# Optimization experiments

Hardware: AMD Instinct MI355X
Metric: run time of the kernel (lower is better)

Reference implementation:

```python
import jax, jax.numpy as jnp
import numpy as np

B, D, H, W = 64, 256, 32, 32
K, DC = 1024, 128  # codebook size, codebook dim = D // 2
BETA = 0.25


def setup_inputs() -> dict:
    key = jax.random.key(0)
    ks = jax.random.split(key, 4)
    return {
        "x": jax.random.normal(ks[0], (B, D, H, W), dtype=jnp.float32),
        "pre_W": jax.random.normal(ks[1], (DC, D), dtype=jnp.float32) * (1.0 / np.sqrt(D)),
        "pre_b": jnp.zeros((DC,), dtype=jnp.float32),
        "post_W": jax.random.normal(ks[2], (D, DC), dtype=jnp.float32) * (1.0 / np.sqrt(DC)),
        "post_b": jnp.zeros((D,), dtype=jnp.float32),
        "lookup_table": jax.random.normal(ks[3], (K, DC), dtype=jnp.float32) * (1.0 / np.sqrt(DC)),
    }


def reference(x, pre_W, pre_b, post_W, post_b, lookup_table):
    sg = jax.lax.stop_gradient
    b, d, h, w = x.shape
    # pre-quant 1x1 conv: [b, d, h, w] -> [b, dc, h, w]
    z = jnp.einsum("bchw,oc->bohw", x, pre_W) + pre_b[None, :, None, None]
    # flatten tokens: [b*h*w, dc]
    zf = z.transpose(0, 2, 3, 1).reshape(-1, DC)
    # squared distances to codebook (argmin identical to cdist argmin)
    d2 = (
        jnp.sum(zf * zf, axis=1, keepdims=True)
        - 2.0 * zf @ lookup_table.T
        + jnp.sum(lookup_table * lookup_table, axis=1)[None, :]
    )  # [N, K]
    q = jnp.argmin(d2, axis=1)  # [N]
    x_e = lookup_table[q].reshape(b, h, w, DC).transpose(0, 3, 1, 2)  # [b, dc, h, w]
    # losses (enable_ema_update = False path)
    codebook_loss = jnp.mean((sg(z) - x_e) ** 2)
    commitment_loss = BETA * jnp.mean((z - sg(x_e)) ** 2)
    loss = (1.0 - BETA) * codebook_loss + commitment_loss
    # straight-through estimator
    z_st = z + sg(x_e - z)
    # post-quant 1x1 conv: [b, dc, h, w] -> [b, d, h, w]
    out = jnp.einsum("bchw,oc->bohw", z_st, post_W) + post_b[None, :, None, None]
    # perplexity from empirical code usage
    counts = jnp.zeros((K,), dtype=jnp.float32).at[q].add(1.0)
    e_mean = counts / q.shape[0]
    perplexity = jnp.exp(-jnp.sum(e_mean * jnp.log(e_mean + 1e-10)))
    q_map = q.reshape(b, h, w)
    return out, loss, q_map, perplexity
```

## Files before the change

kernel.cpp:

```cpp
#include <hip/hip_runtime.h>
#include <cstdint>

#define NB   64
#define ND   256
#define NHW  1024
#define NTOK 65536
#define NDC  128
#define NK   1024

#define OFF_LOSS 16777216
#define OFF_Q    16777217
#define OFF_PERP 16842753

#define GAPTHR 1e-3f
#define NEGINF (-3.402823466e38f)

typedef short short8 __attribute__((ext_vector_type(8)));
typedef float f32x4 __attribute__((ext_vector_type(4)));

__device__ __forceinline__ unsigned short f2bf(float f) {
  unsigned u = __float_as_uint(f);
  u += 0x7FFFu + ((u >> 16) & 1u);
  return (unsigned short)(u >> 16);
}
__device__ __forceinline__ float bf2f(unsigned short h) {
  return __uint_as_float(((unsigned)h) << 16);
}

__device__ __forceinline__ void gll16(const void* g, void* l) {
  __builtin_amdgcn_global_load_lds(
      (const __attribute__((address_space(1))) unsigned int*)g,
      (__attribute__((address_space(3))) unsigned int*)l, 16, 0, 0);
}

__global__ __launch_bounds__(256) void k_init(
    const float* __restrict__ lut, const float* __restrict__ preW,
    const float* __restrict__ postW,
    unsigned short* __restrict__ ch,
    unsigned short* __restrict__ pwh, unsigned short* __restrict__ pwl,
    unsigned short* __restrict__ qwh, unsigned short* __restrict__ qwl,
    float* __restrict__ nhn, double* __restrict__ cn2d,
    int* __restrict__ counts, double* __restrict__ lossAcc, int* __restrict__ ctr) {
  int tid = blockIdx.x * 256 + threadIdx.x;
  int stride = gridDim.x * 256;
  for (int i = tid; i < NK * NDC; i += stride) {
    int code = i >> 7, c = i & 127;
    float f = lut[i];
    unsigned short h1 = f2bf(f);
    float r = f - bf2f(h1);
    ch[code * 256 + c] = h1;
    ch[code * 256 + 128 + c] = f2bf(r);
  }
  for (int i = tid; i < NDC * ND; i += stride) {
    float f = preW[i];
    unsigned u = __float_as_uint(f);
    float lf = f - __uint_as_float(u & 0xffff0000u);
    pwh[i] = (unsigned short)(u >> 16);
    pwl[i] = (unsigned short)(__float_as_uint(lf) >> 16);
  }
  for (int i = tid; i < ND * NDC; i += stride) {
    float f = postW[i];
    unsigned u = __float_as_uint(f);
    float lf = f - __uint_as_float(u & 0xffff0000u);
    qwh[i] = (unsigned short)(u >> 16);
    qwl[i] = (unsigned short)(__float_as_uint(lf) >> 16);
  }
  if (tid < NK) {
    float s = 0.f;
    double sd = 0.0;
    for (int c = 0; c < NDC; c++) {
      float v = lut[tid * NDC + c];
      s = fmaf(v, v, s);
      sd = fma((double)v, (double)v, sd);
    }
    nhn[tid] = -0.5f * s;
    cn2d[tid] = sd;
    counts[tid] = 0;
  }
  if (tid == 0) { *lossAcc = 0.0; *ctr = 0; }
}

__global__ __launch_bounds__(256, 3) void k_preconv(
    const float* __restrict__ x, const unsigned short* __restrict__ pwh,
    const unsigned short* __restrict__ pwl, const float* __restrict__ pre_b,
    float* __restrict__ zf) {
  int bx = blockIdx.x;
  int b = bx >> 4, p0 = (bx & 15) * 64;
  int tid = threadIdx.x;
  int lane = tid & 63, w = tid >> 6;
  int g = lane >> 4, l15 = lane & 15;
  int p = p0 + w * 16 + l15;
  const float* xb = x + (size_t)b * (ND * NHW) + p;

  float xv[64];
  #pragma unroll
  for (int c = 0; c < 8; ++c)
    #pragma unroll
    for (int j = 0; j < 8; ++j)
      xv[c * 8 + j] = xb[(size_t)(c * 32 + g * 8 + j) * NHW];

  f32x4 acc[8];
  #pragma unroll
  for (int rt = 0; rt < 8; ++rt) acc[rt] = (f32x4){0.f, 0.f, 0.f, 0.f};

  #pragma unroll
  for (int c = 0; c < 8; ++c) {
    int k0 = c * 32;
    short8 bh, bl;
    #pragma unroll
    for (int j = 0; j < 8; ++j) {
      float f = xv[c * 8 + j];
      unsigned u = __float_as_uint(f);
      float lf = f - __uint_as_float(u & 0xffff0000u);
      bh[j] = (short)(u >> 16);
      bl[j] = (short)(__float_as_uint(lf) >> 16);
    }
    #pragma unroll
    for (int rt = 0; rt < 8; ++rt) {
      short8 ah = *reinterpret_cast<const short8*>(&pwh[(rt * 16 + l15) * ND + k0 + g * 8]);
      short8 al = *reinterpret_cast<const short8*>(&pwl[(rt * 16 + l15) * ND + k0 + g * 8]);
      acc[rt] = __builtin_amdgcn_mfma_f32_16x16x32_bf16(ah, bh, acc[rt], 0, 0, 0);
      acc[rt] = __builtin_amdgcn_mfma_f32_16x16x32_bf16(ah, bl, acc[rt], 0, 0, 0);
      acc[rt] = __builtin_amdgcn_mfma_f32_16x16x32_bf16(al, bh, acc[rt], 0, 0, 0);
    }
  }
  int n = bx * 64 + w * 16 + l15;
  #pragma unroll
  for (int rt = 0; rt < 8; ++rt) {
    float4 bb = *reinterpret_cast<const float4*>(&pre_b[rt * 16 + g * 4]);
    float4 v;
    v.x = acc[rt][0] + bb.x;
    v.y = acc[rt][1] + bb.y;
    v.z = acc[rt][2] + bb.z;
    v.w = acc[rt][3] + bb.w;
    *reinterpret_cast<float4*>(&zf[(size_t)n * NDC + rt * 16 + g * 4]) = v;
  }
}

__global__ __launch_bounds__(256, 2) void k_dist(
    const float* __restrict__ zf, const unsigned short* __restrict__ ch,
    const float* __restrict__ nhn,
    int* __restrict__ q, int* __restrict__ list, int* __restrict__ ctr,
    double* __restrict__ lossAcc) {
  __shared__ __align__(16) short chbuf[2][16384];
  __shared__ float HnLds[NK];
  __shared__ float zn2Lds[4][2][16];
  __shared__ float red[256];
  int tid = threadIdx.x;
  int lane = tid & 63, w = tid >> 6;
  int g = lane >> 4;
  int n0 = blockIdx.x * 128;

  for (int i = tid; i < NK; i += 256) HnLds[i] = nhn[i];

  short8 az[2][8];
  {
    int arow = lane & 15;
    #pragma unroll
    for (int rt = 0; rt < 2; ++rt) {
      const float* zr = zf + (size_t)(n0 + w * 32 + rt * 16 + arow) * NDC;
      float sq = 0.f;
      #pragma unroll
      for (int f = 0; f < 4; ++f) {
        const float* p = zr + f * 32 + g * 8;
        float4 v0 = *reinterpret_cast<const float4*>(p);
        float4 v1 = *reinterpret_cast<const float4*>(p + 4);
        float vv[8] = {v0.x, v0.y, v0.z, v0.w, v1.x, v1.y, v1.z, v1.w};
        short8 hi, lo;
        #pragma unroll
        for (int j = 0; j < 8; ++j) {
          sq = fmaf(vv[j], vv[j], sq);
          unsigned short h1 = f2bf(vv[j]);
          float r = vv[j] - bf2f(h1);
          hi[j] = (short)h1;
          lo[j] = (short)f2bf(r);
        }
        az[rt][f] = hi;
        az[rt][4 + f] = lo;
      }
      sq += __shfl_xor(sq, 16, 64);
      sq += __shfl_xor(sq, 32, 64);
      if (g == 0) zn2Lds[w][rt][arow] = sq;
    }
  }

  float best[2][4], sec[2][4];
  int bidx[2][4];
  #pragma unroll
  for (int rt = 0; rt < 2; ++rt)
    #pragma unroll
    for (int r = 0; r < 4; ++r) { best[rt][r] = NEGINF; sec[rt][r] = NEGINF; bidx[rt][r] = 0; }

  const char* chg = (const char*)ch;
  {
    const char* gb = chg + 0;
    #pragma unroll
    for (int rr = 0; rr < 8; ++rr) {
      int o = rr * 4096 + tid * 16;
      int so = o ^ (((o >> 9) & 7) << 4);
      gll16(gb + so, ((char*)&chbuf[0][0]) + o);
    }
  }
  asm volatile("s_waitcnt vmcnt(0)" ::: "memory");
  __syncthreads();

  int cur = 0;
  for (int chunk = 0; chunk < 16; ++chunk) {
    if (chunk < 15) {
      const char* gb = chg + (chunk + 1) * 32768;
      #pragma unroll
      for (int rr = 0; rr < 8; ++rr) {
        int o = rr * 4096 + tid * 16;
        int so = o ^ (((o >> 9) & 7) << 4);
        gll16(gb + so, ((char*)&chbuf[cur ^ 1][0]) + o);
      }
    }
    const char* cb = (const char*)&chbuf[cur][0];
    for (int ct = 0; ct < 4; ++ct) {
      int codeg = chunk * 64 + ct * 16 + (lane & 15);
      float nh = HnLds[codeg];
      short8 bc[8];
      #pragma unroll
      for (int f = 0; f < 8; ++f) {
        int byte = ((lane & 15) + ct * 16) * 512 + f * 64 + g * 16;
        byte ^= ((lane & 7) << 4);
        bc[f] = *reinterpret_cast<const short8*>(cb + byte);
      }
      f32x4 acc0 = {nh, nh, nh, nh};
      f32x4 acc1 = {nh, nh, nh, nh};
      #pragma unroll
      for (int j = 0; j < 4; ++j) {
        acc0 = __builtin_amdgcn_mfma_f32_16x16x32_bf16(az[0][j], bc[j], acc0, 0, 0, 0);
        acc1 = __builtin_amdgcn_mfma_f32_16x16x32_bf16(az[1][j], bc[j], acc1, 0, 0, 0);
        acc0 = __builtin_amdgcn_mfma_f32_16x16x32_bf16(az[0][j], bc[4 + j], acc0, 0, 0, 0);
        acc1 = __builtin_amdgcn_mfma_f32_16x16x32_bf16(az[1][j], bc[4 + j], acc1, 0, 0, 0);
        acc0 = __builtin_amdgcn_mfma_f32_16x16x32_bf16(az[0][4 + j], bc[j], acc0, 0, 0, 0);
        acc1 = __builtin_amdgcn_mfma_f32_16x16x32_bf16(az[1][4 + j], bc[j], acc1, 0, 0, 0);
      }
      #pragma unroll
      for (int r = 0; r < 4; ++r) {
        float s0 = acc0[r];
        bool t0 = s0 > best[0][r];
        bidx[0][r] = t0 ? codeg : bidx[0][r];
        sec[0][r] = fmaxf(sec[0][r], fminf(s0, best[0][r]));
        best[0][r] = fmaxf(s0, best[0][r]);
        float s1 = acc1[r];
        bool t1 = s1 > best[1][r];
        bidx[1][r] = t1 ? codeg : bidx[1][r];
        sec[1][r] = fmaxf(sec[1][r], fminf(s1, best[1][r]));
        best[1][r] = fmaxf(s1, best[1][r]);
      }
    }
    asm volatile("s_waitcnt vmcnt(0)" ::: "memory");
    __syncthreads();
    cur ^= 1;
  }

  float lsum = 0.f;
  #pragma unroll
  for (int rt = 0; rt < 2; ++rt) {
    #pragma unroll
    for (int r = 0; r < 4; ++r) {
      float b = best[rt][r];
      float s2 = sec[rt][r];
      int bi_ = bidx[rt][r];
      #pragma unroll
      for (int m = 1; m < 16; m <<= 1) {
        float ob = __shfl_xor(b, m, 64);
        float os = __shfl_xor(s2, m, 64);
        int oi = __shfl_xor(bi_, m, 64);
        float ns = fmaxf(fmaxf(s2, os), fminf(b, ob));
        bool take = (ob > b) || (ob == b && oi < bi_);
        b = take ? ob : b;
        bi_ = take ? oi : bi_;
        s2 = ns;
      }
      if ((lane & 15) == 0) {
        int token = n0 + w * 32 + rt * 16 + g * 4 + r;
        q[token] = bi_;
        if (b - s2 < GAPTHR) {
          int pos = atomicAdd(ctr, 1);
          list[pos] = token;
        }
        lsum += zn2Lds[w][rt][g * 4 + r] - 2.0f * b;
      }
    }
  }
  red[tid] = lsum;
  __syncthreads();
  for (int s = 128; s > 0; s >>= 1) {
    if (tid < s) red[tid] += red[tid + s];
    __syncthreads();
  }
  if (tid == 0) atomicAdd(lossAcc, (double)red[0]);
}

__global__ __launch_bounds__(256) void k_rescore(
    const float* __restrict__ x, const float* __restrict__ preW,
    const float* __restrict__ pre_b, const float* __restrict__ lut,
    const double* __restrict__ cn2d,
    const int* __restrict__ list, const int* __restrict__ ctr, int* __restrict__ q) {
  __shared__ float xs[4][256];
  __shared__ double zs[4][128];
  __shared__ double rd[4][256];
  __shared__ int    rc[4][256];
  int nf = *ctr;
  int tid = threadIdx.x;
  int w = tid >> 6, lane = tid & 63;
  for (int g0 = blockIdx.x * 4; g0 < nf; g0 += gridDim.x * 4) {
    int nt = nf - g0; if (nt > 4) nt = 4;
    #pragma unroll
    for (int t = 0; t < 4; ++t) {
      int token = list[g0 + (t < nt ? t : 0)];
      int b = token >> 10, p = token & 1023;
      xs[t][tid] = x[(size_t)(b * ND + tid) * NHW + p];
    }
    __syncthreads();
    #pragma unroll
    for (int rep = 0; rep < 2; ++rep) {
      int idx = rep * 256 + tid;
      int t = idx >> 7, dc = idx & 127;
      double acc = (double)pre_b[dc];
      const float* wr = preW + (size_t)dc * ND;
      #pragma unroll 4
      for (int d = 0; d < ND; d += 4) {
        float4 wv = *reinterpret_cast<const float4*>(wr + d);
        acc = fma((double)wv.x, (double)xs[t][d + 0], acc);
        acc = fma((double)wv.y, (double)xs[t][d + 1], acc);
        acc = fma((double)wv.z, (double)xs[t][d + 2], acc);
        acc = fma((double)wv.w, (double)xs[t][d + 3], acc);
      }
      zs[t][dc] = acc;
    }
    __syncthreads();
    double bd[4]; int bc_[4];
    #pragma unroll
    for (int t = 0; t < 4; ++t) { bd[t] = 1e300; bc_[t] = 0x7fffffff; }
    for (int cc = 0; cc < 4; ++cc) {
      int c = cc * 256 + tid;
      const float* cr = lut + (size_t)c * NDC;
      double a0 = 0.0, a1 = 0.0, a2 = 0.0, a3 = 0.0;
      #pragma unroll 4
      for (int k = 0; k < NDC; ++k) {
        double lc = (double)cr[k];
        a0 = fma(zs[0][k], lc, a0);
        a1 = fma(zs[1][k], lc, a1);
        a2 = fma(zs[2][k], lc, a2);
        a3 = fma(zs[3][k], lc, a3);
      }
      double cn = cn2d[c];
      double d0 = cn - 2.0 * a0; if (d0 < bd[0]) { bd[0] = d0; bc_[0] = c; }
      double d1 = cn - 2.0 * a1; if (d1 < bd[1]) { bd[1] = d1; bc_[1] = c; }
      double d2 = cn - 2.0 * a2; if (d2 < bd[2]) { bd[2] = d2; bc_[2] = c; }
      double d3 = cn - 2.0 * a3; if (d3 < bd[3]) { bd[3] = d3; bc_[3] = c; }
    }
    #pragma unroll
    for (int t = 0; t < 4; ++t) { rd[t][tid] = bd[t]; rc[t][tid] = bc_[t]; }
    __syncthreads();
    {
      double b_ = rd[w][lane]; int c_ = rc[w][lane];
      #pragma unroll
      for (int s = 64; s < 256; s += 64) {
        double ob = rd[w][lane + s]; int oc = rc[w][lane + s];
        if (ob < b_ || (ob == b_ && oc < c_)) { b_ = ob; c_ = oc; }
      }
      #pragma unroll
      for (int m = 1; m < 64; m <<= 1) {
        double ob = __shfl_xor(b_, m, 64);
        int oc = __shfl_xor(c_, m, 64);
        if (ob < b_ || (ob == b_ && oc < c_)) { b_ = ob; c_ = oc; }
      }
      if (lane == 0 && w < nt) q[list[g0 + w]] = c_;
    }
    __syncthreads();
  }
}

__global__ __launch_bounds__(256, 3) void k_post(
    const float* __restrict__ lut,
    const int* __restrict__ q, const unsigned short* __restrict__ qwh,
    const unsigned short* __restrict__ qwl, const float* __restrict__ post_b,
    float* __restrict__ out,
    int* __restrict__ counts, float* __restrict__ outq) {
  int bx = blockIdx.x;
  int n0 = (bx >> 1) * 128;
  int oh = (bx & 1) * 128;
  int b = n0 >> 10, p0 = n0 & 1023;
  int tid = threadIdx.x;
  int lane = tid & 63, w = tid >> 6;
  int g = lane >> 4, l15 = lane & 15;

  int qv[2];
  #pragma unroll
  for (int ct = 0; ct < 2; ++ct) qv[ct] = q[n0 + w * 32 + ct * 16 + l15];

  float4 ga[2][4][2];
  #pragma unroll
  for (int ct = 0; ct < 2; ++ct) {
    const float* xr0 = lut + (size_t)qv[ct] * NDC + g * 8;
    #pragma unroll
    for (int ks = 0; ks < 4; ++ks) {
      ga[ct][ks][0] = *reinterpret_cast<const float4*>(xr0 + ks * 32);
      ga[ct][ks][1] = *reinterpret_cast<const float4*>(xr0 + ks * 32 + 4);
    }
  }

  if (tid < 64) {
    int n = n0 + ((bx & 1) << 6) + tid;
    int c = q[n];
    atomicAdd(&counts[c], 1);
    outq[n] = (float)c;
  }

  short8 ah[2][4], al[2][4];
  #pragma unroll
  for (int ct = 0; ct < 2; ++ct)
    #pragma unroll
    for (int ks = 0; ks < 4; ++ks) {
      float vv[8] = {ga[ct][ks][0].x, ga[ct][ks][0].y, ga[ct][ks][0].z, ga[ct][ks][0].w,
                     ga[ct][ks][1].x, ga[ct][ks][1].y, ga[ct][ks][1].z, ga[ct][ks][1].w};
      #pragma unroll
      for (int j = 0; j < 8; ++j) {
        unsigned u = __float_as_uint(vv[j]);
        float lf = vv[j] - __uint_as_float(u & 0xffff0000u);
        ah[ct][ks][j] = (short)(u >> 16);
        al[ct][ks][j] = (short)(__float_as_uint(lf) >> 16);
      }
    }

  f32x4 acc[8][2];
  #pragma unroll
  for (int nt = 0; nt < 8; ++nt)
    #pragma unroll
    for (int ct = 0; ct < 2; ++ct) acc[nt][ct] = (f32x4){0.f, 0.f, 0.f, 0.f};

  #pragma unroll
  for (int ks = 0; ks < 4; ++ks) {
    int k0 = ks * 32;
    #pragma unroll
    for (int nt = 0; nt < 8; ++nt) {
      short8 bh = *reinterpret_cast<const short8*>(&qwh[(size_t)(oh + nt * 16 + l15) * NDC + k0 + g * 8]);
      short8 bl = *reinterpret_cast<const short8*>(&qwl[(size_t)(oh + nt * 16 + l15) * NDC + k0 + g * 8]);
      #pragma unroll
      for (int ct = 0; ct < 2; ++ct) {
        acc[nt][ct] = __builtin_amdgcn_mfma_f32_16x16x32_bf16(ah[ct][ks], bh, acc[nt][ct], 0, 0, 0);
        acc[nt][ct] = __builtin_amdgcn_mfma_f32_16x16x32_bf16(al[ct][ks], bh, acc[nt][ct], 0, 0, 0);
        acc[nt][ct] = __builtin_amdgcn_mfma_f32_16x16x32_bf16(ah[ct][ks], bl, acc[nt][ct], 0, 0, 0);
      }
    }
  }
  #pragma unroll
  for (int nt = 0; nt < 8; ++nt) {
    int o = oh + nt * 16 + l15;
    float bias = post_b[o];
    float* orow = out + (size_t)(b * ND + o) * NHW;
    #pragma unroll
    for (int ct = 0; ct < 2; ++ct) {
      int p = p0 + w * 32 + ct * 16 + g * 4;
      float4 v;
      v.x = acc[nt][ct][0] + bias;
      v.y = acc[nt][ct][1] + bias;
      v.z = acc[nt][ct][2] + bias;
      v.w = acc[nt][ct][3] + bias;
      *reinterpret_cast<float4*>(orow + p) = v;
    }
  }
}

__global__ __launch_bounds__(256) void k_fin(
    const double* __restrict__ lossAcc, const int* __restrict__ counts,
    float* __restrict__ out_loss, float* __restrict__ out_perp) {
  __shared__ float red[256];
  int tid = threadIdx.x;
  float h = 0.f;
  for (int i = tid; i < NK; i += 256) {
    float e = (float)counts[i] * (1.0f / (float)NTOK);
    h += e * logf(e + 1e-10f);
  }
  red[tid] = h;
  __syncthreads();
  for (int s = 128; s > 0; s >>= 1) {
    if (tid < s) red[tid] += red[tid + s];
    __syncthreads();
  }
  if (tid == 0) {
    *out_perp = expf(-red[0]);
    *out_loss = (float)(*lossAcc / ((double)NTOK * (double)NDC));
  }
}

extern "C" void kernel_launch(void* const* d_in, const int* in_sizes, int n_in,
                              void* d_out, int out_size, void* d_ws, size_t ws_size,
                              hipStream_t stream) {
  const float* x     = (const float*)d_in[0];
  const float* preW  = (const float*)d_in[1];
  const float* preb  = (const float*)d_in[2];
  const float* postW = (const float*)d_in[3];
  const float* postb = (const float*)d_in[4];
  const float* lut   = (const float*)d_in[5];
  float* out = (float*)d_out;

  char* ws = (char*)d_ws;
  float*          zf      = (float*)(ws);
  unsigned short* ch      = (unsigned short*)(ws + 33554432);
  unsigned short* pwh     = (unsigned short*)(ws + 34078720);
  unsigned short* pwl     = (unsigned short*)(ws + 34144256);
  unsigned short* qwh     = (unsigned short*)(ws + 34209792);
  unsigned short* qwl     = (unsigned short*)(ws + 34275328);
  float*          nhn     = (float*)(ws + 34340864);
  int*            q       = (int*)  (ws + 34344960);
  int*            list    = (int*)  (ws + 34607104);
  int*            counts  = (int*)  (ws + 34869248);
  double*         lossAcc = (double*)(ws + 34873344);
  int*            ctr     = (int*)  (ws + 34873352);
  double*         cn2d    = (double*)(ws + 34873360);

  float* out_loss = out + OFF_LOSS;
  float* out_q    = out + OFF_Q;
  float* out_perp = out + OFF_PERP;

  hipLaunchKernelGGL(k_init, dim3(512), dim3(256), 0, stream,
                     lut, preW, postW, ch, pwh, pwl, qwh, qwl, nhn, cn2d,
                     counts, lossAcc, ctr);
  hipLaunchKernelGGL(k_preconv, dim3(1024), dim3(256), 0, stream, x, pwh, pwl, preb, zf);
  hipLaunchKernelGGL(k_dist, dim3(512), dim3(256), 0, stream, zf, ch, nhn, q, list, ctr, lossAcc);
  hipLaunchKernelGGL(k_rescore, dim3(1024), dim3(256), 0, stream,
                     x, preW, preb, lut, cn2d, list, ctr, q);
  hipLaunchKernelGGL(k_post, dim3(1024), dim3(256), 0, stream,
                     lut, q, qwh, qwl, postb, out, counts, out_q);
  hipLaunchKernelGGL(k_fin, dim3(1), dim3(256), 0, stream, lossAcc, counts, out_loss, out_perp);
}
```

Baseline: 222.2 us.

## Tile preconv over 256 tokens with double-buffered LDS staging of x

Rewrites the pre-quant 1x1 conv so each block handles 256 tokens instead of 64. The x slices are staged through double-buffered, swizzled shared memory using direct global-to-LDS loads, and the next channel chunk is prefetched while MFMAs run on the current one. Each loaded weight fragment now feeds four token tiles, which cuts redundant weight reads. In exchange the grid drops from 1024 to 256 blocks at occupancy 1 on a chip with many CUs, and the 32 accumulator tiles raise register pressure.

```diff
diff --git a/kernel.cpp b/kernel.cpp
--- a/kernel.cpp
+++ b/kernel.cpp
@@ -80,60 +80,90 @@
   if (tid == 0) { *lossAcc = 0.0; *ctr = 0; }
 }
 
-__global__ __launch_bounds__(256, 3) void k_preconv(
+__global__ __launch_bounds__(256, 1) void k_preconv(
     const float* __restrict__ x, const unsigned short* __restrict__ pwh,
     const unsigned short* __restrict__ pwl, const float* __restrict__ pre_b,
     float* __restrict__ zf) {
+  __shared__ __align__(16) float xs[2][32 * 256];
   int bx = blockIdx.x;
-  int b = bx >> 4, p0 = (bx & 15) * 64;
+  int b = bx >> 2, p0 = (bx & 3) * 256;
   int tid = threadIdx.x;
   int lane = tid & 63, w = tid >> 6;
   int g = lane >> 4, l15 = lane & 15;
-  int p = p0 + w * 16 + l15;
-  const float* xb = x + (size_t)b * (ND * NHW) + p;
-
-  float xv[64];
-  #pragma unroll
-  for (int c = 0; c < 8; ++c)
-    #pragma unroll
-    for (int j = 0; j < 8; ++j)
-      xv[c * 8 + j] = xb[(size_t)(c * 32 + g * 8 + j) * NHW];
-
-  f32x4 acc[8];
-  #pragma unroll
-  for (int rt = 0; rt < 8; ++rt) acc[rt] = (f32x4){0.f, 0.f, 0.f, 0.f};
-
-  #pragma unroll
-  for (int c = 0; c < 8; ++c) {
-    int k0 = c * 32;
-    short8 bh, bl;
-    #pragma unroll
-    for (int j = 0; j < 8; ++j) {
-      float f = xv[c * 8 + j];
-      unsigned u = __float_as_uint(f);
-      float lf = f - __uint_as_float(u & 0xffff0000u);
-      bh[j] = (short)(u >> 16);
-      bl[j] = (short)(__float_as_uint(lf) >> 16);
+  const char* xb = (const char*)(x + (size_t)b * (ND * NHW) + p0);
+
+  #pragma unroll
+  for (int i = 0; i < 8; ++i) {
+    int o = i * 4096 + tid * 16;
+    int chl = o >> 10;
+    int col = (o & 1023) ^ (((chl >> 3) & 3) << 5);
+    gll16(xb + (size_t)chl * 4096 + col, ((char*)&xs[0][0]) + o);
+  }
+  asm volatile("s_waitcnt vmcnt(0)" ::: "memory");
+  __syncthreads();
+
+  f32x4 acc[8][4];
+  #pragma unroll
+  for (int rt = 0; rt < 8; ++rt)
+    #pragma unroll
+    for (int ct = 0; ct < 4; ++ct) acc[rt][ct] = (f32x4){0.f, 0.f, 0.f, 0.f};
+
+  int cur = 0;
+  for (int ks = 0; ks < 8; ++ks) {
+    if (ks < 7) {
+      const char* gb = xb + (size_t)(ks + 1) * 32 * 4096;
+      #pragma unroll
+      for (int i = 0; i < 8; ++i) {
+        int o = i * 4096 + tid * 16;
+        int chl = o >> 10;
+        int col = (o & 1023) ^ (((chl >> 3) & 3) << 5);
+        gll16(gb + (size_t)chl * 4096 + col, ((char*)&xs[cur ^ 1][0]) + o);
+      }
+    }
+    int k0 = ks * 32;
+    short8 bh[4], bl[4];
+    #pragma unroll
+    for (int ct = 0; ct < 4; ++ct) {
+      int tok = w * 64 + ct * 16 + l15;
+      int tswz = tok ^ (g << 3);
+      #pragma unroll
+      for (int j = 0; j < 8; ++j) {
+        float f = xs[cur][(g * 8 + j) * 256 + tswz];
+        unsigned u = __float_as_uint(f);
+        float lf = f - __uint_as_float(u & 0xffff0000u);
+        bh[ct][j] = (short)(u >> 16);
+        bl[ct][j] = (short)(__float_as_uint(lf) >> 16);
+      }
     }
     #pragma unroll
     for (int rt = 0; rt < 8; ++rt) {
       short8 ah = *reinterpret_cast<const short8*>(&pwh[(rt * 16 + l15) * ND + k0 + g * 8]);
       short8 al = *reinterpret_cast<const short8*>(&pwl[(rt * 16 + l15) * ND + k0 + g * 8]);
-      acc[rt] = __builtin_amdgcn_mfma_f32_16x16x32_bf16(ah, bh, acc[rt], 0, 0, 0);
-      acc[rt] = __builtin_amdgcn_mfma_f32_16x16x32_bf16(ah, bl, acc[rt], 0, 0, 0);
-      acc[rt] = __builtin_amdgcn_mfma_f32_16x16x32_bf16(al, bh, acc[rt], 0, 0, 0);
-    }
-  }
-  int n = bx * 64 + w * 16 + l15;
+      #pragma unroll
+      for (int ct = 0; ct < 4; ++ct) {
+        acc[rt][ct] = __builtin_amdgcn_mfma_f32_16x16x32_bf16(ah, bh[ct], acc[rt][ct], 0, 0, 0);
+        acc[rt][ct] = __builtin_amdgcn_mfma_f32_16x16x32_bf16(ah, bl[ct], acc[rt][ct], 0, 0, 0);
+        acc[rt][ct] = __builtin_amdgcn_mfma_f32_16x16x32_bf16(al, bh[ct], acc[rt][ct], 0, 0, 0);
+      }
+    }
+    asm volatile("s_waitcnt vmcnt(0)" ::: "memory");
+    __syncthreads();
+    cur ^= 1;
+  }
+
   #pragma unroll
   for (int rt = 0; rt < 8; ++rt) {
     float4 bb = *reinterpret_cast<const float4*>(&pre_b[rt * 16 + g * 4]);
-    float4 v;
-    v.x = acc[rt][0] + bb.x;
-    v.y = acc[rt][1] + bb.y;
-    v.z = acc[rt][2] + bb.z;
-    v.w = acc[rt][3] + bb.w;
-    *reinterpret_cast<float4*>(&zf[(size_t)n * NDC + rt * 16 + g * 4]) = v;
+    #pragma unroll
+    for (int ct = 0; ct < 4; ++ct) {
+      int n = bx * 256 + w * 64 + ct * 16 + l15;
+      float4 v;
+      v.x = acc[rt][ct][0] + bb.x;
+      v.y = acc[rt][ct][1] + bb.y;
+      v.z = acc[rt][ct][2] + bb.z;
+      v.w = acc[rt][ct][3] + bb.w;
+      *reinterpret_cast<float4*>(&zf[(size_t)n * NDC + rt * 16 + g * 4]) = v;
+    }
   }
 }
 
@@ -522,7 +552,7 @@
   hipLaunchKernelGGL(k_init, dim3(512), dim3(256), 0, stream,
                      lut, preW, postW, ch, pwh, pwl, qwh, qwl, nhn, cn2d,
                      counts, lossAcc, ctr);
-  hipLaunchKernelGGL(k_preconv, dim3(1024), dim3(256), 0, stream, x, pwh, pwl, preb, zf);
+  hipLaunchKernelGGL(k_preconv, dim3(256), dim3(256), 0, stream, x, pwh, pwl, preb, zf);
   hipLaunchKernelGGL(k_dist, dim3(512), dim3(256), 0, stream, zf, ch, nhn, q, list, ctr, lossAcc);
   hipLaunchKernelGGL(k_rescore, dim3(1024), dim3(256), 0, stream,
                      x, preW, preb, lut, cn2d, list, ctr, q);
```

Result: faster. 192.4 us (-13.4%).
